# Kernel tuning notes

Measured on AMD Instinct MI355X. Metric: run time of the kernel, lower is better.

The kernel has to match this reference:

```python
import jax, jax.numpy as jnp
import numpy as np

SOS_INDEX = 1  # args.sos_index
EOS_INDEX = 2  # args.eos_index

V, H, T, B = 32000, 1024, 32, 64


def setup_inputs() -> dict:
    key = jax.random.key(0)
    ks = jax.random.split(key, 10)
    s = 0.05  # weight scale to keep softmax/tanh in a sane range
    return {
        "E": jax.random.normal(ks[0], (V, H), jnp.float32) * s,          # embedding table
        "W_ih": jax.random.normal(ks[1], (4 * H, H), jnp.float32) * s,   # LSTMCell input weights (i,f,g,o)
        "W_hh": jax.random.normal(ks[2], (4 * H, H), jnp.float32) * s,
        "b_ih": jax.random.normal(ks[3], (4 * H,), jnp.float32) * s,
        "b_hh": jax.random.normal(ks[4], (4 * H,), jnp.float32) * s,
        "W_out": jax.random.normal(ks[5], (V, H), jnp.float32) * s,      # self.out Linear
        "b_out": jnp.zeros((V,), jnp.float32),
        "encoder_hidden": jax.random.normal(ks[6], (B, H), jnp.float32),
        "encoder_cell": jax.random.normal(ks[7], (B, H), jnp.float32),
        "target_var": jax.random.randint(ks[8], (T, B), 0, V),
        "target_max_len": T,
    }


def reference(E, W_ih, W_hh, b_ih, b_hh, W_out, b_out,
              encoder_hidden, encoder_cell, target_var, target_max_len):
    # Eval-mode decode: use_teacher_forcing = False -> greedy argmax feedback.
    batch = encoder_hidden.shape[0]
    x0 = E[jnp.full((batch,), SOS_INDEX)]  # embedding(SOS) for every batch element

    def step(carry, _):
        x, h, c = carry
        # PyTorch LSTMCell: gates ordered (i, f, g, o)
        gates = x @ W_ih.T + b_ih + h @ W_hh.T + b_hh      # [B, 4H]
        i, f, g, o = jnp.split(gates, 4, axis=1)
        c_new = jax.nn.sigmoid(f) * c + jax.nn.sigmoid(i) * jnp.tanh(g)
        h_new = jax.nn.sigmoid(o) * jnp.tanh(c_new)
        logits = h_new @ W_out.T + b_out                    # [B, V]
        mask = jax.nn.softmax(logits, axis=1)[:, EOS_INDEX] # [B]
        # greedy feedback: topk(1) == argmax
        x_next = E[jnp.argmax(logits, axis=1)]              # [B, H]
        return (x_next, h_new, c_new), (logits, mask)

    _, (outputs, masks) = jax.lax.scan(
        step, (x0, encoder_hidden, encoder_cell), None, length=target_max_len)
    return outputs, masks  # [T, B, V], [T, B]
```

## Files before the change

### kernel.cpp

```cpp
#include <hip/hip_runtime.h>
#include <math.h>


typedef short bf16x8 __attribute__((ext_vector_type(8)));
typedef float f32x4 __attribute__((ext_vector_type(4)));

constexpr int kH = 1024;
constexpr int kFH = 4096;
constexpr int kB = 64;
constexpr int kV = 32000;
constexpr int kT = 32;
constexpr int kSOS = 1;
constexpr int kEOS = 2;

__device__ inline unsigned short f2bf(float f) {
  unsigned int u = __float_as_uint(f);
  u += 0x7fffu + ((u >> 16) & 1u);
  return (unsigned short)(u >> 16);
}
__device__ inline float bf2f(unsigned short h) {
  return __uint_as_float(((unsigned int)h) << 16);
}

__global__ __launch_bounds__(256) void init_kernel(
    const float* __restrict__ E, const float* __restrict__ eh,
    const float* __restrict__ ec, float* __restrict__ ws) {
  int g = blockIdx.x * 256 + threadIdx.x;
  int u = g >> 6, b = g & 63;
  float* x = ws;
  float* h = ws + 65536;
  float* c = ws + 131072;
  x[g] = E[(size_t)kSOS * kH + u];
  h[u * 64 + b] = eh[(size_t)b * kH + u];
  c[u * 64 + b] = ec[(size_t)b * kH + u];
}

__global__ __launch_bounds__(256) void wsplit_kernel(
    const float* __restrict__ W, unsigned short* __restrict__ hi,
    unsigned short* __restrict__ lo) {
  size_t i = ((size_t)blockIdx.x * 256 + threadIdx.x) * 4;
  float4 w = *(const float4*)(W + i);
  unsigned short h0 = f2bf(w.x), h1 = f2bf(w.y), h2 = f2bf(w.z), h3 = f2bf(w.w);
  ushort4 hv = make_ushort4(h0, h1, h2, h3);
  ushort4 lv = make_ushort4(f2bf(w.x - bf2f(h0)), f2bf(w.y - bf2f(h1)),
                            f2bf(w.z - bf2f(h2)), f2bf(w.w - bf2f(h3)));
  *(ushort4*)(hi + i) = hv;
  *(ushort4*)(lo + i) = lv;
}

__global__ __launch_bounds__(256) void gates_kernel(
    const float* __restrict__ Wih, const float* __restrict__ Whh,
    const float* __restrict__ x, const float* __restrict__ h,
    float* __restrict__ part) {
  __shared__ __align__(16) float Wt[64 * 68];
  __shared__ __align__(16) float Zt[64 * 68];
  const int tid = threadIdx.x;
  const int s = blockIdx.y;
  const int r0 = blockIdx.x * 64;
  const int phase = s >> 2;
  const int kc0 = (s & 3) * 256;
  const float* __restrict__ W = phase ? Whh : Wih;
  const float* __restrict__ z = phase ? h : x;
  const int tb4 = tid & 15;
  const int tr4 = tid >> 4;
  float acc[4][4];
#pragma unroll
  for (int i = 0; i < 4; ++i)
#pragma unroll
    for (int j = 0; j < 4; ++j) acc[i][j] = 0.f;

  for (int kc = kc0; kc < kc0 + 256; kc += 64) {
#pragma unroll
    for (int l = 0; l < 4; ++l) {
      int f4 = tid + 256 * l;
      int row = f4 >> 4;
      int c4 = f4 & 15;
      float4 w = *(const float4*)(W + (size_t)(r0 + row) * kH + kc + c4 * 4);
      float wv[4] = {w.x, w.y, w.z, w.w};
#pragma unroll
      for (int cc = 0; cc < 4; ++cc) {
        int c = (cc + c4) & 3;
        Wt[(c4 * 4 + c) * 68 + row] = wv[c];
      }
    }
#pragma unroll
    for (int l = 0; l < 4; ++l) {
      int f4 = tid + 256 * l;
      int kk = f4 >> 4;
      int b4 = f4 & 15;
      *(float4*)(&Zt[kk * 68 + b4 * 4]) =
          *(const float4*)(z + (size_t)(kc + kk) * 64 + b4 * 4);
    }
    __syncthreads();
#pragma unroll
    for (int kk = 0; kk < 64; ++kk) {
      float4 a = *(const float4*)(&Wt[kk * 68 + tr4 * 4]);
      float4 zb = *(const float4*)(&Zt[kk * 68 + tb4 * 4]);
      float av[4] = {a.x, a.y, a.z, a.w};
      float zv[4] = {zb.x, zb.y, zb.z, zb.w};
#pragma unroll
      for (int i = 0; i < 4; ++i)
#pragma unroll
        for (int j = 0; j < 4; ++j) acc[i][j] += av[i] * zv[j];
    }
    __syncthreads();
  }
#pragma unroll
  for (int i = 0; i < 4; ++i) {
    float4 o = make_float4(acc[i][0], acc[i][1], acc[i][2], acc[i][3]);
    *(float4*)(&part[((size_t)s * kFH + r0 + tr4 * 4 + i) * 64 + tb4 * 4]) = o;
  }
}

__global__ __launch_bounds__(256) void lstm_kernel(
    const float* __restrict__ part, const float* __restrict__ bih,
    const float* __restrict__ bhh, float* __restrict__ h,
    float* __restrict__ c, unsigned short* __restrict__ Hhi,
    unsigned short* __restrict__ Hlo) {
  int g = blockIdx.x * 256 + threadIdx.x;
  int b = g & 63, u = g >> 6;
  float gate[4];
#pragma unroll
  for (int ty = 0; ty < 4; ++ty) {
    int r = ty * kH + u;
    float acc = bih[r] + bhh[r];
#pragma unroll
    for (int s2 = 0; s2 < 8; ++s2)
      acc += part[((size_t)s2 * kFH + r) * 64 + b];
    gate[ty] = acc;
  }
  float gi = 1.f / (1.f + expf(-gate[0]));
  float gf = 1.f / (1.f + expf(-gate[1]));
  float gg = tanhf(gate[2]);
  float go = 1.f / (1.f + expf(-gate[3]));
  float cn = gf * c[g] + gi * gg;
  float hn = go * tanhf(cn);
  c[g] = cn;
  h[g] = hn;
  unsigned short hb = f2bf(hn);
  Hhi[(size_t)b * kH + u] = hb;
  Hlo[(size_t)b * kH + u] = f2bf(hn - bf2f(hb));
}

struct Frags {
  bf16x8 ah[2], al[2], bh[4], bl[4];
};

__device__ inline void load_frags(Frags& f, const unsigned short* wp0,
                                  const unsigned short* wp1,
                                  const unsigned short* lp0,
                                  const unsigned short* lp1,
                                  const unsigned short* hh,
                                  const unsigned short* hl, int ko) {
  f.ah[0] = *(const bf16x8*)(wp0 + ko);
  f.ah[1] = *(const bf16x8*)(wp1 + ko);
  f.al[0] = *(const bf16x8*)(lp0 + ko);
  f.al[1] = *(const bf16x8*)(lp1 + ko);
#pragma unroll
  for (int bt = 0; bt < 4; ++bt) {
    f.bh[bt] = *(const bf16x8*)(hh + bt * 16 * kH + ko);
    f.bl[bt] = *(const bf16x8*)(hl + bt * 16 * kH + ko);
  }
}

__device__ inline void do_mfma(const Frags& f, f32x4 acc[2][4]) {
#pragma unroll
  for (int tv = 0; tv < 2; ++tv)
#pragma unroll
    for (int bt = 0; bt < 4; ++bt) {
      acc[tv][bt] = __builtin_amdgcn_mfma_f32_16x16x32_bf16(
          f.ah[tv], f.bh[bt], acc[tv][bt], 0, 0, 0);
      acc[tv][bt] = __builtin_amdgcn_mfma_f32_16x16x32_bf16(
          f.ah[tv], f.bl[bt], acc[tv][bt], 0, 0, 0);
      acc[tv][bt] = __builtin_amdgcn_mfma_f32_16x16x32_bf16(
          f.al[tv], f.bh[bt], acc[tv][bt], 0, 0, 0);
    }
}

__global__ __launch_bounds__(256) void logits_mfma_kernel(
    const unsigned short* __restrict__ Whi, const unsigned short* __restrict__ Wlo,
    const unsigned short* __restrict__ Hhi, const unsigned short* __restrict__ Hlo,
    const float* __restrict__ bout, float* __restrict__ out,
    float* __restrict__ pmax_g, float* __restrict__ psum_g,
    int* __restrict__ pidx_g) {
  const int tid = threadIdx.x;
  const int wave = tid >> 6, lane = tid & 63;
  const int m = lane & 15, q = lane >> 4;
  const int v0 = blockIdx.x * 128 + wave * 32;
  const unsigned short* wp0 = Whi + (size_t)(v0 + m) * kH + q * 8;
  const unsigned short* wp1 = Whi + (size_t)(v0 + 16 + m) * kH + q * 8;
  const unsigned short* lp0 = Wlo + (size_t)(v0 + m) * kH + q * 8;
  const unsigned short* lp1 = Wlo + (size_t)(v0 + 16 + m) * kH + q * 8;
  const unsigned short* hh = Hhi + (size_t)m * kH + q * 8;
  const unsigned short* hl = Hlo + (size_t)m * kH + q * 8;

  f32x4 acc[2][4];
#pragma unroll
  for (int tv = 0; tv < 2; ++tv)
#pragma unroll
    for (int bt = 0; bt < 4; ++bt) acc[tv][bt] = (f32x4){0.f, 0.f, 0.f, 0.f};

  Frags f0, f1;
  load_frags(f0, wp0, wp1, lp0, lp1, hh, hl, 0);
  for (int kc = 0; kc < kH; kc += 64) {
    if (kc + 32 < kH) load_frags(f1, wp0, wp1, lp0, lp1, hh, hl, kc + 32);
    do_mfma(f0, acc);
    if (kc + 64 < kH) load_frags(f0, wp0, wp1, lp0, lp1, hh, hl, kc + 64);
    do_mfma(f1, acc);
  }

  float4 bo0 = *(const float4*)(bout + v0 + q * 4);
  float4 bo1 = *(const float4*)(bout + v0 + 16 + q * 4);
#pragma unroll
  for (int tv = 0; tv < 2; ++tv) {
    float4 bo = tv ? bo1 : bo0;
#pragma unroll
    for (int bt = 0; bt < 4; ++bt) {
      int b = bt * 16 + m;
      f32x4 a = acc[tv][bt];
      a[0] += bo.x; a[1] += bo.y; a[2] += bo.z; a[3] += bo.w;
      acc[tv][bt] = a;
      float4 o = make_float4(a[0], a[1], a[2], a[3]);
      *(float4*)(out + (size_t)b * kV + v0 + tv * 16 + q * 4) = o;
    }
  }

  __shared__ float lred[4][4][64];
  __shared__ int lidx[4][4][64];
  __shared__ float bbm[64];
  const int blk = blockIdx.x;
  const int vbase = blk * 128;

#pragma unroll
  for (int bt = 0; bt < 4; ++bt) {
    float pmv = -INFINITY;
    int piv = 0x7fffffff;
#pragma unroll
    for (int tv = 0; tv < 2; ++tv)
#pragma unroll
      for (int r = 0; r < 4; ++r) {
        float val = acc[tv][bt][r];
        int v = vbase + wave * 32 + tv * 16 + q * 4 + r;
        if (val > pmv) { pmv = val; piv = v; }
      }
    lred[wave][q][bt * 16 + m] = pmv;
    lidx[wave][q][bt * 16 + m] = piv;
  }
  __syncthreads();
  if (tid < 64) {
    float bm = -INFINITY;
    int bi = 0x7fffffff;
#pragma unroll
    for (int w = 0; w < 4; ++w)
#pragma unroll
      for (int qq = 0; qq < 4; ++qq) {
        float v2 = lred[w][qq][tid];
        int i2 = lidx[w][qq][tid];
        if (v2 > bm || (v2 == bm && i2 < bi)) { bm = v2; bi = i2; }
      }
    bbm[tid] = bm;
    pmax_g[(size_t)tid * 256 + blk] = bm;
    pidx_g[(size_t)tid * 256 + blk] = bi;
  }
  __syncthreads();
#pragma unroll
  for (int bt = 0; bt < 4; ++bt) {
    float bm = bbm[bt * 16 + m];
    float s = 0.f;
#pragma unroll
    for (int tv = 0; tv < 2; ++tv)
#pragma unroll
      for (int r = 0; r < 4; ++r) s += expf(acc[tv][bt][r] - bm);
    lred[wave][q][bt * 16 + m] = s;
  }
  __syncthreads();
  if (tid < 64) {
    float s = 0.f;
#pragma unroll
    for (int w = 0; w < 4; ++w)
#pragma unroll
      for (int qq = 0; qq < 4; ++qq) s += lred[w][qq][tid];
    psum_g[(size_t)tid * 256 + blk] = s;
  }
}

__global__ __launch_bounds__(256) void finalize_kernel(
    const float* __restrict__ pm, const float* __restrict__ ps,
    const int* __restrict__ pig, const float* __restrict__ out_t,
    const float* __restrict__ E, float* __restrict__ x,
    float* __restrict__ mask) {
  __shared__ float sm[256];
  __shared__ int si[256];
  __shared__ float ss[256];
  const int b = blockIdx.x, tid = threadIdx.x;
  float m = -INFINITY;
  int idx = 0x7fffffff;
  if (tid < 250) {
    m = pm[(size_t)b * 256 + tid];
    idx = pig[(size_t)b * 256 + tid];
  }
  sm[tid] = m;
  si[tid] = idx;
  __syncthreads();
  for (int off = 128; off > 0; off >>= 1) {
    if (tid < off) {
      float o = sm[tid + off];
      int oi = si[tid + off];
      if (o > sm[tid] || (o == sm[tid] && oi < si[tid])) {
        sm[tid] = o;
        si[tid] = oi;
      }
    }
    __syncthreads();
  }
  const float M = sm[0];
  const int amax = si[0];
  float term = 0.f;
  if (tid < 250) term = ps[(size_t)b * 256 + tid] * expf(m - M);
  ss[tid] = term;
  __syncthreads();
  for (int off = 128; off > 0; off >>= 1) {
    if (tid < off) ss[tid] += ss[tid + off];
    __syncthreads();
  }
  if (tid == 0) mask[b] = expf(out_t[(size_t)b * kV + kEOS] - M) / ss[0];
  for (int u = tid; u < kH; u += 256)
    x[(size_t)u * 64 + b] = E[(size_t)amax * kH + u];
}

extern "C" void kernel_launch(void* const* d_in, const int* in_sizes, int n_in,
                              void* d_out, int out_size, void* d_ws,
                              size_t ws_size, hipStream_t stream) {
  const float* E = (const float*)d_in[0];
  const float* Wih = (const float*)d_in[1];
  const float* Whh = (const float*)d_in[2];
  const float* bih = (const float*)d_in[3];
  const float* bhh = (const float*)d_in[4];
  const float* Wout = (const float*)d_in[5];
  const float* bout = (const float*)d_in[6];
  const float* eh = (const float*)d_in[7];
  const float* ec = (const float*)d_in[8];
  float* out = (float*)d_out;
  float* ws = (float*)d_ws;

  float* x = ws;
  float* h = ws + 65536;
  float* c = ws + 131072;
  float* part = ws + 196608;
  float* pmaxg = ws + 2293760;
  float* psumg = ws + 2310144;
  int* pidxg = (int*)(ws + 2326528);
  unsigned short* Whi = (unsigned short*)(ws + 2359296);
  unsigned short* Wlo = Whi + (size_t)kV * kH;
  unsigned short* Hhi = Wlo + (size_t)kV * kH;
  unsigned short* Hlo = Hhi + (size_t)kB * kH;

  init_kernel<<<256, 256, 0, stream>>>(E, eh, ec, ws);
  wsplit_kernel<<<kV, 256, 0, stream>>>(Wout, Whi, Wlo);
  for (int t = 0; t < kT; ++t) {
    float* out_t = out + (size_t)t * kB * kV;
    gates_kernel<<<dim3(64, 8), 256, 0, stream>>>(Wih, Whh, x, h, part);
    lstm_kernel<<<256, 256, 0, stream>>>(part, bih, bhh, h, c, Hhi, Hlo);
    logits_mfma_kernel<<<250, 256, 0, stream>>>(Whi, Wlo, Hhi, Hlo, bout,
                                                out_t, pmaxg, psumg, pidxg);
    finalize_kernel<<<64, 256, 0, stream>>>(pmaxg, psumg, pidxg, out_t, E, x,
                                            out + (size_t)kT * kB * kV + t * kB);
  }
}
```

Measured before the change: 2.972 ms.

## Fuse gate GEMM with LSTM cell and fold finalize into logits via last-block reduction

After: 5.239 ms. +76.3%, slower.

```diff
diff --git a/kernel.cpp b/kernel.cpp
--- a/kernel.cpp
+++ b/kernel.cpp
@@ -6,7 +6,6 @@
 typedef float f32x4 __attribute__((ext_vector_type(4)));
 
 constexpr int kH = 1024;
-constexpr int kFH = 4096;
 constexpr int kB = 64;
 constexpr int kV = 32000;
 constexpr int kT = 32;
@@ -23,16 +22,22 @@
 }
 
 __global__ __launch_bounds__(256) void init_kernel(
-    const float* __restrict__ E, const float* __restrict__ eh,
-    const float* __restrict__ ec, float* __restrict__ ws) {
+    const float* __restrict__ eh, const float* __restrict__ ec,
+    float* __restrict__ ws) {
   int g = blockIdx.x * 256 + threadIdx.x;
-  int u = g >> 6, b = g & 63;
-  float* x = ws;
-  float* h = ws + 65536;
-  float* c = ws + 131072;
-  x[g] = E[(size_t)kSOS * kH + u];
-  h[u * 64 + b] = eh[(size_t)b * kH + u];
-  c[u * 64 + b] = ec[(size_t)b * kH + u];
+  float* c = ws;
+  float* hT0 = ws + 65536;
+  int* counter = (int*)(ws + 245760);
+  int* amax = (int*)(ws + 245824);
+  if (g < 65536) {
+    int u = g >> 6, b = g & 63;
+    c[u * 64 + b] = ec[(size_t)b * kH + u];
+  } else {
+    int i = g - 65536;
+    hT0[i] = eh[i];
+  }
+  if (g < 64) amax[g] = kSOS;
+  if (g == 64) *counter = 0;
 }
 
 __global__ __launch_bounds__(256) void wsplit_kernel(
@@ -48,95 +53,88 @@
   *(ushort4*)(lo + i) = lv;
 }
 
-__global__ __launch_bounds__(256) void gates_kernel(
+__global__ __launch_bounds__(256) void recur_kernel(
     const float* __restrict__ Wih, const float* __restrict__ Whh,
-    const float* __restrict__ x, const float* __restrict__ h,
-    float* __restrict__ part) {
-  __shared__ __align__(16) float Wt[64 * 68];
-  __shared__ __align__(16) float Zt[64 * 68];
-  const int tid = threadIdx.x;
-  const int s = blockIdx.y;
-  const int r0 = blockIdx.x * 64;
-  const int phase = s >> 2;
-  const int kc0 = (s & 3) * 256;
-  const float* __restrict__ W = phase ? Whh : Wih;
-  const float* __restrict__ z = phase ? h : x;
-  const int tb4 = tid & 15;
-  const int tr4 = tid >> 4;
-  float acc[4][4];
-#pragma unroll
-  for (int i = 0; i < 4; ++i)
-#pragma unroll
-    for (int j = 0; j < 4; ++j) acc[i][j] = 0.f;
-
-  for (int kc = kc0; kc < kc0 + 256; kc += 64) {
-#pragma unroll
-    for (int l = 0; l < 4; ++l) {
-      int f4 = tid + 256 * l;
-      int row = f4 >> 4;
-      int c4 = f4 & 15;
-      float4 w = *(const float4*)(W + (size_t)(r0 + row) * kH + kc + c4 * 4);
-      float wv[4] = {w.x, w.y, w.z, w.w};
-#pragma unroll
-      for (int cc = 0; cc < 4; ++cc) {
-        int c = (cc + c4) & 3;
-        Wt[(c4 * 4 + c) * 68 + row] = wv[c];
-      }
-    }
-#pragma unroll
-    for (int l = 0; l < 4; ++l) {
-      int f4 = tid + 256 * l;
-      int kk = f4 >> 4;
-      int b4 = f4 & 15;
-      *(float4*)(&Zt[kk * 68 + b4 * 4]) =
-          *(const float4*)(z + (size_t)(kc + kk) * 64 + b4 * 4);
-    }
-    __syncthreads();
-#pragma unroll
-    for (int kk = 0; kk < 64; ++kk) {
-      float4 a = *(const float4*)(&Wt[kk * 68 + tr4 * 4]);
-      float4 zb = *(const float4*)(&Zt[kk * 68 + tb4 * 4]);
-      float av[4] = {a.x, a.y, a.z, a.w};
-      float zv[4] = {zb.x, zb.y, zb.z, zb.w};
-#pragma unroll
-      for (int i = 0; i < 4; ++i)
-#pragma unroll
-        for (int j = 0; j < 4; ++j) acc[i][j] += av[i] * zv[j];
-    }
-    __syncthreads();
-  }
-#pragma unroll
-  for (int i = 0; i < 4; ++i) {
-    float4 o = make_float4(acc[i][0], acc[i][1], acc[i][2], acc[i][3]);
-    *(float4*)(&part[((size_t)s * kFH + r0 + tr4 * 4 + i) * 64 + tb4 * 4]) = o;
-  }
-}
-
-__global__ __launch_bounds__(256) void lstm_kernel(
-    const float* __restrict__ part, const float* __restrict__ bih,
-    const float* __restrict__ bhh, float* __restrict__ h,
+    const float* __restrict__ E, const float* __restrict__ bih,
+    const float* __restrict__ bhh, const int* __restrict__ amax,
+    const float* __restrict__ hTprev, float* __restrict__ hTnext,
     float* __restrict__ c, unsigned short* __restrict__ Hhi,
     unsigned short* __restrict__ Hlo) {
-  int g = blockIdx.x * 256 + threadIdx.x;
-  int b = g & 63, u = g >> 6;
+  __shared__ __align__(16) float Wt[16 * 132];
+  __shared__ __align__(16) float Zt[64 * 132];
+  __shared__ const float* rowp[64];
+  const int tid = threadIdx.x;
+  const int u0 = blockIdx.x * 4;
+  const int rg = tid >> 6;
+  const int b = tid & 63;
+
+  if (tid < 64) rowp[tid] = E + (size_t)amax[tid] * kH;
+  __syncthreads();
+
+  f32x4 acc[4];
+#pragma unroll
+  for (int j = 0; j < 4; ++j) acc[j] = (f32x4){0.f, 0.f, 0.f, 0.f};
+
+  f32x4 wreg[2], zreg[8];
+  auto prefetch = [&](int cidx) {
+    const int ph = cidx >> 3;
+    const int kc = (cidx & 7) * 128;
+    const float* __restrict__ Wb = ph ? Whh : Wih;
+#pragma unroll
+    for (int l = 0; l < 2; ++l) {
+      int s = tid + 256 * l, ri = s >> 5, kq = s & 31;
+      size_t grow = (size_t)((ri >> 2) * kH + u0 + (ri & 3));
+      wreg[l] = *(const f32x4*)(Wb + grow * kH + kc + kq * 4);
+    }
+#pragma unroll
+    for (int l = 0; l < 8; ++l) {
+      int s = tid + 256 * l, zb = s >> 5, kq = s & 31;
+      const float* zp = ph ? (hTprev + (size_t)zb * kH) : rowp[zb];
+      zreg[l] = *(const f32x4*)(zp + kc + kq * 4);
+    }
+  };
+
+  prefetch(0);
+  for (int cidx = 0; cidx < 16; ++cidx) {
+#pragma unroll
+    for (int l = 0; l < 2; ++l) {
+      int s = tid + 256 * l;
+      *(f32x4*)(&Wt[(s >> 5) * 132 + (s & 31) * 4]) = wreg[l];
+    }
+#pragma unroll
+    for (int l = 0; l < 8; ++l) {
+      int s = tid + 256 * l;
+      *(f32x4*)(&Zt[(s >> 5) * 132 + (s & 31) * 4]) = zreg[l];
+    }
+    __syncthreads();
+    if (cidx < 15) prefetch(cidx + 1);
+    const float* ztb = Zt + b * 132;
+    const float* wtb = Wt + rg * 132;
+#pragma unroll
+    for (int k4 = 0; k4 < 32; ++k4) {
+      f32x4 z4 = *(const f32x4*)(ztb + k4 * 4);
+      acc[0] += (*(const f32x4*)(wtb + k4 * 4)) * z4;
+      acc[1] += (*(const f32x4*)(wtb + 528 + k4 * 4)) * z4;
+      acc[2] += (*(const f32x4*)(wtb + 1056 + k4 * 4)) * z4;
+      acc[3] += (*(const f32x4*)(wtb + 1584 + k4 * 4)) * z4;
+    }
+    __syncthreads();
+  }
+
+  const int u = u0 + rg;
   float gate[4];
 #pragma unroll
-  for (int ty = 0; ty < 4; ++ty) {
-    int r = ty * kH + u;
-    float acc = bih[r] + bhh[r];
-#pragma unroll
-    for (int s2 = 0; s2 < 8; ++s2)
-      acc += part[((size_t)s2 * kFH + r) * 64 + b];
-    gate[ty] = acc;
-  }
+  for (int j = 0; j < 4; ++j)
+    gate[j] = acc[j][0] + acc[j][1] + acc[j][2] + acc[j][3] + bih[j * kH + u] +
+              bhh[j * kH + u];
   float gi = 1.f / (1.f + expf(-gate[0]));
   float gf = 1.f / (1.f + expf(-gate[1]));
   float gg = tanhf(gate[2]);
   float go = 1.f / (1.f + expf(-gate[3]));
-  float cn = gf * c[g] + gi * gg;
+  float cn = gf * c[u * 64 + b] + gi * gg;
   float hn = go * tanhf(cn);
-  c[g] = cn;
-  h[g] = hn;
+  c[u * 64 + b] = cn;
+  hTnext[(size_t)b * kH + u] = hn;
   unsigned short hb = f2bf(hn);
   Hhi[(size_t)b * kH + u] = hb;
   Hlo[(size_t)b * kH + u] = f2bf(hn - bf2f(hb));
@@ -182,7 +180,8 @@
     const unsigned short* __restrict__ Hhi, const unsigned short* __restrict__ Hlo,
     const float* __restrict__ bout, float* __restrict__ out,
     float* __restrict__ pmax_g, float* __restrict__ psum_g,
-    int* __restrict__ pidx_g) {
+    int* __restrict__ pidx_g, int* __restrict__ counter,
+    int* __restrict__ amax_out, float* __restrict__ mask) {
   const int tid = threadIdx.x;
   const int wave = tid >> 6, lane = tid & 63;
   const int m = lane & 15, q = lane >> 4;
@@ -259,8 +258,8 @@
         if (v2 > bm || (v2 == bm && i2 < bi)) { bm = v2; bi = i2; }
       }
     bbm[tid] = bm;
-    pmax_g[(size_t)tid * 256 + blk] = bm;
-    pidx_g[(size_t)tid * 256 + blk] = bi;
+    pmax_g[(size_t)blk * 64 + tid] = bm;
+    pidx_g[(size_t)blk * 64 + tid] = bi;
   }
   __syncthreads();
 #pragma unroll
@@ -280,52 +279,57 @@
     for (int w = 0; w < 4; ++w)
 #pragma unroll
       for (int qq = 0; qq < 4; ++qq) s += lred[w][qq][tid];
-    psum_g[(size_t)tid * 256 + blk] = s;
-  }
-}
-
-__global__ __launch_bounds__(256) void finalize_kernel(
-    const float* __restrict__ pm, const float* __restrict__ ps,
-    const int* __restrict__ pig, const float* __restrict__ out_t,
-    const float* __restrict__ E, float* __restrict__ x,
-    float* __restrict__ mask) {
-  __shared__ float sm[256];
-  __shared__ int si[256];
-  __shared__ float ss[256];
-  const int b = blockIdx.x, tid = threadIdx.x;
-  float m = -INFINITY;
+    psum_g[(size_t)blk * 64 + tid] = s;
+  }
+
+  __shared__ int is_last;
+  __threadfence();
+  __syncthreads();
+  if (tid == 0) is_last = (atomicAdd(counter, 1) == 249);
+  __syncthreads();
+  if (!is_last) return;
+  __threadfence();
+
+  __shared__ float fm[4][64];
+  __shared__ int fi[4][64];
+  __shared__ float fs[4][64];
+  const int qq = tid >> 6, bb = tid & 63;
+  float mx = -INFINITY;
   int idx = 0x7fffffff;
-  if (tid < 250) {
-    m = pm[(size_t)b * 256 + tid];
-    idx = pig[(size_t)b * 256 + tid];
-  }
-  sm[tid] = m;
-  si[tid] = idx;
-  __syncthreads();
-  for (int off = 128; off > 0; off >>= 1) {
-    if (tid < off) {
-      float o = sm[tid + off];
-      int oi = si[tid + off];
-      if (o > sm[tid] || (o == sm[tid] && oi < si[tid])) {
-        sm[tid] = o;
-        si[tid] = oi;
-      }
-    }
-    __syncthreads();
-  }
-  const float M = sm[0];
-  const int amax = si[0];
-  float term = 0.f;
-  if (tid < 250) term = ps[(size_t)b * 256 + tid] * expf(m - M);
-  ss[tid] = term;
-  __syncthreads();
-  for (int off = 128; off > 0; off >>= 1) {
-    if (tid < off) ss[tid] += ss[tid + off];
-    __syncthreads();
-  }
-  if (tid == 0) mask[b] = expf(out_t[(size_t)b * kV + kEOS] - M) / ss[0];
-  for (int u = tid; u < kH; u += 256)
-    x[(size_t)u * 64 + b] = E[(size_t)amax * kH + u];
+  for (int k = qq; k < 250; k += 4) {
+    float v = pmax_g[(size_t)k * 64 + bb];
+    int ii = pidx_g[(size_t)k * 64 + bb];
+    if (v > mx || (v == mx && ii < idx)) { mx = v; idx = ii; }
+  }
+  fm[qq][bb] = mx;
+  fi[qq][bb] = idx;
+  __syncthreads();
+  if (tid < 64) {
+    float M = fm[0][tid];
+    int ai = fi[0][tid];
+#pragma unroll
+    for (int w = 1; w < 4; ++w) {
+      float v = fm[w][tid];
+      int ii = fi[w][tid];
+      if (v > M || (v == M && ii < ai)) { M = v; ai = ii; }
+    }
+    fm[0][tid] = M;
+    fi[0][tid] = ai;
+  }
+  __syncthreads();
+  float M = fm[0][bb];
+  float s = 0.f;
+  for (int k = qq; k < 250; k += 4)
+    s += psum_g[(size_t)k * 64 + bb] * expf(pmax_g[(size_t)k * 64 + bb] - M);
+  fs[qq][bb] = s;
+  __syncthreads();
+  if (tid < 64) {
+    float S = fs[0][tid] + fs[1][tid] + fs[2][tid] + fs[3][tid];
+    float eosl = out[(size_t)tid * kV + kEOS];
+    mask[tid] = expf(eosl - M) / S;
+    amax_out[tid] = fi[0][tid];
+    if (tid == 0) *counter = 0;
+  }
 }
 
 extern "C" void kernel_launch(void* const* d_in, const int* in_sizes, int n_in,
@@ -343,27 +347,29 @@
   float* out = (float*)d_out;
   float* ws = (float*)d_ws;
 
-  float* x = ws;
-  float* h = ws + 65536;
-  float* c = ws + 131072;
-  float* part = ws + 196608;
-  float* pmaxg = ws + 2293760;
-  float* psumg = ws + 2310144;
-  int* pidxg = (int*)(ws + 2326528);
+  float* c = ws;
+  float* hT0 = ws + 65536;
+  float* hT1 = ws + 131072;
+  float* pmaxg = ws + 196608;
+  float* psumg = ws + 212992;
+  int* pidxg = (int*)(ws + 229376);
+  int* counter = (int*)(ws + 245760);
+  int* amax = (int*)(ws + 245824);
   unsigned short* Whi = (unsigned short*)(ws + 2359296);
   unsigned short* Wlo = Whi + (size_t)kV * kH;
   unsigned short* Hhi = Wlo + (size_t)kV * kH;
   unsigned short* Hlo = Hhi + (size_t)kB * kH;
 
-  init_kernel<<<256, 256, 0, stream>>>(E, eh, ec, ws);
+  init_kernel<<<512, 256, 0, stream>>>(eh, ec, ws);
   wsplit_kernel<<<kV, 256, 0, stream>>>(Wout, Whi, Wlo);
   for (int t = 0; t < kT; ++t) {
     float* out_t = out + (size_t)t * kB * kV;
-    gates_kernel<<<dim3(64, 8), 256, 0, stream>>>(Wih, Whh, x, h, part);
-    lstm_kernel<<<256, 256, 0, stream>>>(part, bih, bhh, h, c, Hhi, Hlo);
-    logits_mfma_kernel<<<250, 256, 0, stream>>>(Whi, Wlo, Hhi, Hlo, bout,
-                                                out_t, pmaxg, psumg, pidxg);
-    finalize_kernel<<<64, 256, 0, stream>>>(pmaxg, psumg, pidxg, out_t, E, x,
-                                            out + (size_t)kT * kB * kV + t * kB);
-  }
-}
+    float* hTp = (t & 1) ? hT1 : hT0;
+    float* hTn = (t & 1) ? hT0 : hT1;
+    recur_kernel<<<256, 256, 0, stream>>>(Wih, Whh, E, bih, bhh, amax, hTp,
+                                          hTn, c, Hhi, Hlo);
+    logits_mfma_kernel<<<250, 256, 0, stream>>>(
+        Whi, Wlo, Hhi, Hlo, bout, out_t, pmaxg, psumg, pidxg, counter, amax,
+        out + (size_t)kT * kB * kV + t * kB);
+  }
+}
```

## Fuse argmax/mask finalize into gates kernel and stage H via LDS in logits

Applied to the files above, without the earlier changes.

Result: slower. 3.390 ms (+14.1%).

```diff
diff --git a/kernel.cpp b/kernel.cpp
--- a/kernel.cpp
+++ b/kernel.cpp
@@ -3,6 +3,7 @@
 
 
 typedef short bf16x8 __attribute__((ext_vector_type(8)));
+typedef unsigned short ush8 __attribute__((ext_vector_type(8)));
 typedef float f32x4 __attribute__((ext_vector_type(4)));
 
 constexpr int kH = 1024;
@@ -23,16 +24,19 @@
 }
 
 __global__ __launch_bounds__(256) void init_kernel(
-    const float* __restrict__ E, const float* __restrict__ eh,
-    const float* __restrict__ ec, float* __restrict__ ws) {
+    const float* __restrict__ eh, const float* __restrict__ ec,
+    float* __restrict__ ws) {
   int g = blockIdx.x * 256 + threadIdx.x;
-  int u = g >> 6, b = g & 63;
-  float* x = ws;
   float* h = ws + 65536;
   float* c = ws + 131072;
-  x[g] = E[(size_t)kSOS * kH + u];
-  h[u * 64 + b] = eh[(size_t)b * kH + u];
-  c[u * 64 + b] = ec[(size_t)b * kH + u];
+  if (g < 65536) {
+    int u = g >> 6, b = g & 63;
+    c[u * 64 + b] = ec[(size_t)b * kH + u];
+  } else {
+    int i = g - 65536;
+    int u = i >> 6, b = i & 63;
+    h[i] = eh[(size_t)b * kH + u];
+  }
 }
 
 __global__ __launch_bounds__(256) void wsplit_kernel(
@@ -50,17 +54,67 @@
 
 __global__ __launch_bounds__(256) void gates_kernel(
     const float* __restrict__ Wih, const float* __restrict__ Whh,
-    const float* __restrict__ x, const float* __restrict__ h,
-    float* __restrict__ part) {
+    const float* __restrict__ E, const float* __restrict__ h,
+    float* __restrict__ part, const float* __restrict__ pmax_g,
+    const float* __restrict__ psum_g, const int* __restrict__ pidx_g,
+    const float* __restrict__ out_prev, float* __restrict__ mask_prev, int t) {
   __shared__ __align__(16) float Wt[64 * 68];
   __shared__ __align__(16) float Zt[64 * 68];
+  __shared__ const float* rowp[64];
+  __shared__ float redA[4][64];
+  __shared__ int redI[4][64];
+  __shared__ float redS[4][64];
   const int tid = threadIdx.x;
   const int s = blockIdx.y;
   const int r0 = blockIdx.x * 64;
   const int phase = s >> 2;
   const int kc0 = (s & 3) * 256;
   const float* __restrict__ W = phase ? Whh : Wih;
-  const float* __restrict__ z = phase ? h : x;
+
+  if (!phase) {
+    const int b = tid & 63, kq = tid >> 6;
+    if (t == 0) {
+      if (tid < 64) rowp[tid] = E + (size_t)kSOS * kH;
+    } else {
+      float mx = -INFINITY;
+      int ix = 0x7fffffff;
+      for (int k = kq; k < 250; k += 4) {
+        float v = pmax_g[k * 64 + b];
+        int ii = pidx_g[k * 64 + b];
+        if (v > mx || (v == mx && ii < ix)) { mx = v; ix = ii; }
+      }
+      redA[kq][b] = mx;
+      redI[kq][b] = ix;
+      __syncthreads();
+      if (tid < 64) {
+        float M = redA[0][tid];
+        int ai = redI[0][tid];
+#pragma unroll
+        for (int w2 = 1; w2 < 4; ++w2) {
+          float v = redA[w2][tid];
+          int ii = redI[w2][tid];
+          if (v > M || (v == M && ii < ai)) { M = v; ai = ii; }
+        }
+        rowp[tid] = E + (size_t)ai * kH;
+        redA[0][tid] = M;
+      }
+      if (blockIdx.x == 0) {
+        __syncthreads();
+        float M = redA[0][b];
+        float sacc = 0.f;
+        for (int k = kq; k < 250; k += 4)
+          sacc += psum_g[k * 64 + b] * expf(pmax_g[k * 64 + b] - M);
+        redS[kq][b] = sacc;
+        __syncthreads();
+        if (tid < 64) {
+          float S = redS[0][tid] + redS[1][tid] + redS[2][tid] + redS[3][tid];
+          mask_prev[tid] = expf(out_prev[(size_t)tid * kV + kEOS] - M) / S;
+        }
+      }
+    }
+  }
+  __syncthreads();
+
   const int tb4 = tid & 15;
   const int tr4 = tid >> 4;
   float acc[4][4];
@@ -83,13 +137,24 @@
         Wt[(c4 * 4 + c) * 68 + row] = wv[c];
       }
     }
-#pragma unroll
-    for (int l = 0; l < 4; ++l) {
-      int f4 = tid + 256 * l;
-      int kk = f4 >> 4;
-      int b4 = f4 & 15;
-      *(float4*)(&Zt[kk * 68 + b4 * 4]) =
-          *(const float4*)(z + (size_t)(kc + kk) * 64 + b4 * 4);
+    if (!phase) {
+#pragma unroll
+      for (int l = 0; l < 4; ++l) {
+        int g = tid + 256 * l;
+        int zb = g >> 4, k4 = g & 15;
+        f32x4 v = *(const f32x4*)(rowp[zb] + kc + k4 * 4);
+#pragma unroll
+        for (int j = 0; j < 4; ++j) Zt[(k4 * 4 + j) * 68 + zb] = v[j];
+      }
+    } else {
+#pragma unroll
+      for (int l = 0; l < 4; ++l) {
+        int f4 = tid + 256 * l;
+        int kk = f4 >> 4;
+        int b4 = f4 & 15;
+        *(float4*)(&Zt[kk * 68 + b4 * 4]) =
+            *(const float4*)(h + (size_t)(kc + kk) * 64 + b4 * 4);
+      }
     }
     __syncthreads();
 #pragma unroll
@@ -142,47 +207,13 @@
   Hlo[(size_t)b * kH + u] = f2bf(hn - bf2f(hb));
 }
 
-struct Frags {
-  bf16x8 ah[2], al[2], bh[4], bl[4];
-};
-
-__device__ inline void load_frags(Frags& f, const unsigned short* wp0,
-                                  const unsigned short* wp1,
-                                  const unsigned short* lp0,
-                                  const unsigned short* lp1,
-                                  const unsigned short* hh,
-                                  const unsigned short* hl, int ko) {
-  f.ah[0] = *(const bf16x8*)(wp0 + ko);
-  f.ah[1] = *(const bf16x8*)(wp1 + ko);
-  f.al[0] = *(const bf16x8*)(lp0 + ko);
-  f.al[1] = *(const bf16x8*)(lp1 + ko);
-#pragma unroll
-  for (int bt = 0; bt < 4; ++bt) {
-    f.bh[bt] = *(const bf16x8*)(hh + bt * 16 * kH + ko);
-    f.bl[bt] = *(const bf16x8*)(hl + bt * 16 * kH + ko);
-  }
-}
-
-__device__ inline void do_mfma(const Frags& f, f32x4 acc[2][4]) {
-#pragma unroll
-  for (int tv = 0; tv < 2; ++tv)
-#pragma unroll
-    for (int bt = 0; bt < 4; ++bt) {
-      acc[tv][bt] = __builtin_amdgcn_mfma_f32_16x16x32_bf16(
-          f.ah[tv], f.bh[bt], acc[tv][bt], 0, 0, 0);
-      acc[tv][bt] = __builtin_amdgcn_mfma_f32_16x16x32_bf16(
-          f.ah[tv], f.bl[bt], acc[tv][bt], 0, 0, 0);
-      acc[tv][bt] = __builtin_amdgcn_mfma_f32_16x16x32_bf16(
-          f.al[tv], f.bh[bt], acc[tv][bt], 0, 0, 0);
-    }
-}
-
 __global__ __launch_bounds__(256) void logits_mfma_kernel(
     const unsigned short* __restrict__ Whi, const unsigned short* __restrict__ Wlo,
     const unsigned short* __restrict__ Hhi, const unsigned short* __restrict__ Hlo,
     const float* __restrict__ bout, float* __restrict__ out,
     float* __restrict__ pmax_g, float* __restrict__ psum_g,
     int* __restrict__ pidx_g) {
+  __shared__ __align__(16) unsigned short Hs[8192];
   const int tid = threadIdx.x;
   const int wave = tid >> 6, lane = tid & 63;
   const int m = lane & 15, q = lane >> 4;
@@ -191,8 +222,16 @@
   const unsigned short* wp1 = Whi + (size_t)(v0 + 16 + m) * kH + q * 8;
   const unsigned short* lp0 = Wlo + (size_t)(v0 + m) * kH + q * 8;
   const unsigned short* lp1 = Wlo + (size_t)(v0 + 16 + m) * kH + q * 8;
-  const unsigned short* hh = Hhi + (size_t)m * kH + q * 8;
-  const unsigned short* hl = Hlo + (size_t)m * kH + q * 8;
+
+  const unsigned short* sptr[4];
+  int sdst[4];
+#pragma unroll
+  for (int l = 0; l < 4; ++l) {
+    int g = tid + 256 * l;
+    int tile = g >> 9, row = (g >> 3) & 63, cg = g & 7;
+    sptr[l] = (tile ? Hlo : Hhi) + (size_t)row * kH + cg * 8;
+    sdst[l] = tile * 4096 + row * 64 + ((cg ^ (row & 7)) * 8);
+  }
 
   f32x4 acc[2][4];
 #pragma unroll
@@ -200,13 +239,59 @@
 #pragma unroll
     for (int bt = 0; bt < 4; ++bt) acc[tv][bt] = (f32x4){0.f, 0.f, 0.f, 0.f};
 
-  Frags f0, f1;
-  load_frags(f0, wp0, wp1, lp0, lp1, hh, hl, 0);
+  struct WF { bf16x8 ah[2], al[2]; };
+  WF w0, w1;
+  ush8 hreg[4];
+
+  auto loadW = [&](WF& f, int ko) {
+    f.ah[0] = *(const bf16x8*)(wp0 + ko);
+    f.ah[1] = *(const bf16x8*)(wp1 + ko);
+    f.al[0] = *(const bf16x8*)(lp0 + ko);
+    f.al[1] = *(const bf16x8*)(lp1 + ko);
+  };
+  auto loadH = [&](int kc) {
+#pragma unroll
+    for (int l = 0; l < 4; ++l) hreg[l] = *(const ush8*)(sptr[l] + kc);
+  };
+  auto readHfrag = [&](bf16x8 bh[4], bf16x8 bl[4], int koff) {
+    int gbase = q + (koff >> 3);
+#pragma unroll
+    for (int bt = 0; bt < 4; ++bt) {
+      int row = bt * 16 + m;
+      int off = row * 64 + ((gbase ^ (row & 7)) * 8);
+      bh[bt] = *(const bf16x8*)(Hs + off);
+      bl[bt] = *(const bf16x8*)(Hs + 4096 + off);
+    }
+  };
+  auto mfma3 = [&](const WF& f, bf16x8 bh[4], bf16x8 bl[4]) {
+#pragma unroll
+    for (int tv = 0; tv < 2; ++tv)
+#pragma unroll
+      for (int bt = 0; bt < 4; ++bt) {
+        acc[tv][bt] = __builtin_amdgcn_mfma_f32_16x16x32_bf16(
+            f.ah[tv], bh[bt], acc[tv][bt], 0, 0, 0);
+        acc[tv][bt] = __builtin_amdgcn_mfma_f32_16x16x32_bf16(
+            f.ah[tv], bl[bt], acc[tv][bt], 0, 0, 0);
+        acc[tv][bt] = __builtin_amdgcn_mfma_f32_16x16x32_bf16(
+            f.al[tv], bh[bt], acc[tv][bt], 0, 0, 0);
+      }
+  };
+
+  loadH(0);
+  loadW(w0, 0);
   for (int kc = 0; kc < kH; kc += 64) {
-    if (kc + 32 < kH) load_frags(f1, wp0, wp1, lp0, lp1, hh, hl, kc + 32);
-    do_mfma(f0, acc);
-    if (kc + 64 < kH) load_frags(f0, wp0, wp1, lp0, lp1, hh, hl, kc + 64);
-    do_mfma(f1, acc);
+    __syncthreads();
+#pragma unroll
+    for (int l = 0; l < 4; ++l) *(ush8*)(Hs + sdst[l]) = hreg[l];
+    __syncthreads();
+    if (kc + 64 < kH) loadH(kc + 64);
+    bf16x8 bh[4], bl[4];
+    loadW(w1, kc + 32);
+    readHfrag(bh, bl, 0);
+    mfma3(w0, bh, bl);
+    if (kc + 64 < kH) loadW(w0, kc + 64);
+    readHfrag(bh, bl, 32);
+    mfma3(w1, bh, bl);
   }
 
   float4 bo0 = *(const float4*)(bout + v0 + q * 4);
@@ -259,8 +344,8 @@
         if (v2 > bm || (v2 == bm && i2 < bi)) { bm = v2; bi = i2; }
       }
     bbm[tid] = bm;
-    pmax_g[(size_t)tid * 256 + blk] = bm;
-    pidx_g[(size_t)tid * 256 + blk] = bi;
+    pmax_g[(size_t)blk * 64 + tid] = bm;
+    pidx_g[(size_t)blk * 64 + tid] = bi;
   }
   __syncthreads();
 #pragma unroll
@@ -280,52 +365,39 @@
     for (int w = 0; w < 4; ++w)
 #pragma unroll
       for (int qq = 0; qq < 4; ++qq) s += lred[w][qq][tid];
-    psum_g[(size_t)tid * 256 + blk] = s;
-  }
-}
-
-__global__ __launch_bounds__(256) void finalize_kernel(
+    psum_g[(size_t)blk * 64 + tid] = s;
+  }
+}
+
+__global__ __launch_bounds__(256) void final_mask_kernel(
     const float* __restrict__ pm, const float* __restrict__ ps,
-    const int* __restrict__ pig, const float* __restrict__ out_t,
-    const float* __restrict__ E, float* __restrict__ x,
-    float* __restrict__ mask) {
-  __shared__ float sm[256];
-  __shared__ int si[256];
-  __shared__ float ss[256];
-  const int b = blockIdx.x, tid = threadIdx.x;
-  float m = -INFINITY;
-  int idx = 0x7fffffff;
-  if (tid < 250) {
-    m = pm[(size_t)b * 256 + tid];
-    idx = pig[(size_t)b * 256 + tid];
-  }
-  sm[tid] = m;
-  si[tid] = idx;
-  __syncthreads();
-  for (int off = 128; off > 0; off >>= 1) {
-    if (tid < off) {
-      float o = sm[tid + off];
-      int oi = si[tid + off];
-      if (o > sm[tid] || (o == sm[tid] && oi < si[tid])) {
-        sm[tid] = o;
-        si[tid] = oi;
-      }
-    }
-    __syncthreads();
-  }
-  const float M = sm[0];
-  const int amax = si[0];
-  float term = 0.f;
-  if (tid < 250) term = ps[(size_t)b * 256 + tid] * expf(m - M);
-  ss[tid] = term;
-  __syncthreads();
-  for (int off = 128; off > 0; off >>= 1) {
-    if (tid < off) ss[tid] += ss[tid + off];
-    __syncthreads();
-  }
-  if (tid == 0) mask[b] = expf(out_t[(size_t)b * kV + kEOS] - M) / ss[0];
-  for (int u = tid; u < kH; u += 256)
-    x[(size_t)u * 64 + b] = E[(size_t)amax * kH + u];
+    const float* __restrict__ out_t, float* __restrict__ mask) {
+  __shared__ float rm[4][64];
+  __shared__ float rs[4][64];
+  const int tid = threadIdx.x;
+  const int b = tid & 63, kq = tid >> 6;
+  float mx = -INFINITY;
+  for (int k = kq; k < 250; k += 4) {
+    float v = pm[k * 64 + b];
+    if (v > mx) mx = v;
+  }
+  rm[kq][b] = mx;
+  __syncthreads();
+  if (tid < 64) {
+    float M = fmaxf(fmaxf(rm[0][tid], rm[1][tid]), fmaxf(rm[2][tid], rm[3][tid]));
+    rm[0][tid] = M;
+  }
+  __syncthreads();
+  float M = rm[0][b];
+  float s = 0.f;
+  for (int k = kq; k < 250; k += 4)
+    s += ps[k * 64 + b] * expf(pm[k * 64 + b] - M);
+  rs[kq][b] = s;
+  __syncthreads();
+  if (tid < 64) {
+    float S = rs[0][tid] + rs[1][tid] + rs[2][tid] + rs[3][tid];
+    mask[tid] = expf(out_t[(size_t)tid * kV + kEOS] - M) / S;
+  }
 }
 
 extern "C" void kernel_launch(void* const* d_in, const int* in_sizes, int n_in,
@@ -343,7 +415,6 @@
   float* out = (float*)d_out;
   float* ws = (float*)d_ws;
 
-  float* x = ws;
   float* h = ws + 65536;
   float* c = ws + 131072;
   float* part = ws + 196608;
@@ -354,16 +425,21 @@
   unsigned short* Wlo = Whi + (size_t)kV * kH;
   unsigned short* Hhi = Wlo + (size_t)kV * kH;
   unsigned short* Hlo = Hhi + (size_t)kB * kH;
-
-  init_kernel<<<256, 256, 0, stream>>>(E, eh, ec, ws);
+  float* maskbase = out + (size_t)kT * kB * kV;
+
+  init_kernel<<<512, 256, 0, stream>>>(eh, ec, ws);
   wsplit_kernel<<<kV, 256, 0, stream>>>(Wout, Whi, Wlo);
   for (int t = 0; t < kT; ++t) {
     float* out_t = out + (size_t)t * kB * kV;
-    gates_kernel<<<dim3(64, 8), 256, 0, stream>>>(Wih, Whh, x, h, part);
+    const float* out_prev = t ? out + (size_t)(t - 1) * kB * kV : nullptr;
+    float* mask_prev = t ? maskbase + (size_t)(t - 1) * kB : nullptr;
+    gates_kernel<<<dim3(64, 8), 256, 0, stream>>>(
+        Wih, Whh, E, h, part, pmaxg, psumg, pidxg, out_prev, mask_prev, t);
     lstm_kernel<<<256, 256, 0, stream>>>(part, bih, bhh, h, c, Hhi, Hlo);
     logits_mfma_kernel<<<250, 256, 0, stream>>>(Whi, Wlo, Hhi, Hlo, bout,
                                                 out_t, pmaxg, psumg, pidxg);
-    finalize_kernel<<<64, 256, 0, stream>>>(pmaxg, psumg, pidxg, out_t, E, x,
-                                            out + (size_t)kT * kB * kV + t * kB);
-  }
-}
+  }
+  final_mask_kernel<<<1, 256, 0, stream>>>(
+      pmaxg, psumg, out + (size_t)(kT - 1) * kB * kV,
+      maskbase + (size_t)(kT - 1) * kB);
+}
```

## Split logits K dimension across two wave groups with LDS reduction

Applied to the files above, without the earlier changes.

After: 3.001 ms. About the same (+1.0%).

```diff
diff --git a/kernel.cpp b/kernel.cpp
--- a/kernel.cpp
+++ b/kernel.cpp
@@ -177,7 +177,7 @@
     }
 }
 
-__global__ __launch_bounds__(256) void logits_mfma_kernel(
+__global__ __launch_bounds__(512, 2) void logits_mfma_kernel(
     const unsigned short* __restrict__ Whi, const unsigned short* __restrict__ Wlo,
     const unsigned short* __restrict__ Hhi, const unsigned short* __restrict__ Hlo,
     const float* __restrict__ bout, float* __restrict__ out,
@@ -185,14 +185,17 @@
     int* __restrict__ pidx_g) {
   const int tid = threadIdx.x;
   const int wave = tid >> 6, lane = tid & 63;
+  const int ws = wave & 3;
+  const int kh = wave >> 2;
   const int m = lane & 15, q = lane >> 4;
-  const int v0 = blockIdx.x * 128 + wave * 32;
-  const unsigned short* wp0 = Whi + (size_t)(v0 + m) * kH + q * 8;
-  const unsigned short* wp1 = Whi + (size_t)(v0 + 16 + m) * kH + q * 8;
-  const unsigned short* lp0 = Wlo + (size_t)(v0 + m) * kH + q * 8;
-  const unsigned short* lp1 = Wlo + (size_t)(v0 + 16 + m) * kH + q * 8;
-  const unsigned short* hh = Hhi + (size_t)m * kH + q * 8;
-  const unsigned short* hl = Hlo + (size_t)m * kH + q * 8;
+  const int v0 = blockIdx.x * 128 + ws * 32;
+  const int koff = kh * 512;
+  const unsigned short* wp0 = Whi + (size_t)(v0 + m) * kH + koff + q * 8;
+  const unsigned short* wp1 = Whi + (size_t)(v0 + 16 + m) * kH + koff + q * 8;
+  const unsigned short* lp0 = Wlo + (size_t)(v0 + m) * kH + koff + q * 8;
+  const unsigned short* lp1 = Wlo + (size_t)(v0 + 16 + m) * kH + koff + q * 8;
+  const unsigned short* hh = Hhi + (size_t)m * kH + koff + q * 8;
+  const unsigned short* hl = Hlo + (size_t)m * kH + koff + q * 8;
 
   f32x4 acc[2][4];
 #pragma unroll
@@ -202,26 +205,49 @@
 
   Frags f0, f1;
   load_frags(f0, wp0, wp1, lp0, lp1, hh, hl, 0);
-  for (int kc = 0; kc < kH; kc += 64) {
-    if (kc + 32 < kH) load_frags(f1, wp0, wp1, lp0, lp1, hh, hl, kc + 32);
+  for (int kc = 0; kc < 512; kc += 64) {
+    if (kc + 32 < 512) load_frags(f1, wp0, wp1, lp0, lp1, hh, hl, kc + 32);
     do_mfma(f0, acc);
-    if (kc + 64 < kH) load_frags(f0, wp0, wp1, lp0, lp1, hh, hl, kc + 64);
+    if (kc + 64 < 512) load_frags(f0, wp0, wp1, lp0, lp1, hh, hl, kc + 64);
     do_mfma(f1, acc);
   }
 
-  float4 bo0 = *(const float4*)(bout + v0 + q * 4);
-  float4 bo1 = *(const float4*)(bout + v0 + 16 + q * 4);
-#pragma unroll
-  for (int tv = 0; tv < 2; ++tv) {
-    float4 bo = tv ? bo1 : bo0;
-#pragma unroll
-    for (int bt = 0; bt < 4; ++bt) {
-      int b = bt * 16 + m;
-      f32x4 a = acc[tv][bt];
-      a[0] += bo.x; a[1] += bo.y; a[2] += bo.z; a[3] += bo.w;
-      acc[tv][bt] = a;
-      float4 o = make_float4(a[0], a[1], a[2], a[3]);
-      *(float4*)(out + (size_t)b * kV + v0 + tv * 16 + q * 4) = o;
+  __shared__ float combf[4][32][65];
+  if (kh == 1) {
+#pragma unroll
+    for (int tv = 0; tv < 2; ++tv)
+#pragma unroll
+      for (int bt = 0; bt < 4; ++bt)
+#pragma unroll
+        for (int r = 0; r < 4; ++r)
+          combf[ws][(tv * 4 + bt) * 4 + r][lane] = acc[tv][bt][r];
+  }
+  __syncthreads();
+  if (kh == 0) {
+#pragma unroll
+    for (int tv = 0; tv < 2; ++tv)
+#pragma unroll
+      for (int bt = 0; bt < 4; ++bt)
+#pragma unroll
+        for (int r = 0; r < 4; ++r)
+          acc[tv][bt][r] += combf[ws][(tv * 4 + bt) * 4 + r][lane];
+  }
+
+  if (kh == 0) {
+    float4 bo0 = *(const float4*)(bout + v0 + q * 4);
+    float4 bo1 = *(const float4*)(bout + v0 + 16 + q * 4);
+#pragma unroll
+    for (int tv = 0; tv < 2; ++tv) {
+      float4 bo = tv ? bo1 : bo0;
+#pragma unroll
+      for (int bt = 0; bt < 4; ++bt) {
+        int b = bt * 16 + m;
+        f32x4 a = acc[tv][bt];
+        a[0] += bo.x; a[1] += bo.y; a[2] += bo.z; a[3] += bo.w;
+        acc[tv][bt] = a;
+        float4 o = make_float4(a[0], a[1], a[2], a[3]);
+        *(float4*)(out + (size_t)b * kV + v0 + tv * 16 + q * 4) = o;
+      }
     }
   }
 
@@ -231,20 +257,22 @@
   const int blk = blockIdx.x;
   const int vbase = blk * 128;
 
-#pragma unroll
-  for (int bt = 0; bt < 4; ++bt) {
-    float pmv = -INFINITY;
-    int piv = 0x7fffffff;
-#pragma unroll
-    for (int tv = 0; tv < 2; ++tv)
-#pragma unroll
-      for (int r = 0; r < 4; ++r) {
-        float val = acc[tv][bt][r];
-        int v = vbase + wave * 32 + tv * 16 + q * 4 + r;
-        if (val > pmv) { pmv = val; piv = v; }
-      }
-    lred[wave][q][bt * 16 + m] = pmv;
-    lidx[wave][q][bt * 16 + m] = piv;
+  if (kh == 0) {
+#pragma unroll
+    for (int bt = 0; bt < 4; ++bt) {
+      float pmv = -INFINITY;
+      int piv = 0x7fffffff;
+#pragma unroll
+      for (int tv = 0; tv < 2; ++tv)
+#pragma unroll
+        for (int r = 0; r < 4; ++r) {
+          float val = acc[tv][bt][r];
+          int v = vbase + ws * 32 + tv * 16 + q * 4 + r;
+          if (val > pmv) { pmv = val; piv = v; }
+        }
+      lred[ws][q][bt * 16 + m] = pmv;
+      lidx[ws][q][bt * 16 + m] = piv;
+    }
   }
   __syncthreads();
   if (tid < 64) {
@@ -263,15 +291,17 @@
     pidx_g[(size_t)tid * 256 + blk] = bi;
   }
   __syncthreads();
-#pragma unroll
-  for (int bt = 0; bt < 4; ++bt) {
-    float bm = bbm[bt * 16 + m];
-    float s = 0.f;
-#pragma unroll
-    for (int tv = 0; tv < 2; ++tv)
-#pragma unroll
-      for (int r = 0; r < 4; ++r) s += expf(acc[tv][bt][r] - bm);
-    lred[wave][q][bt * 16 + m] = s;
+  if (kh == 0) {
+#pragma unroll
+    for (int bt = 0; bt < 4; ++bt) {
+      float bm = bbm[bt * 16 + m];
+      float s = 0.f;
+#pragma unroll
+      for (int tv = 0; tv < 2; ++tv)
+#pragma unroll
+        for (int r = 0; r < 4; ++r) s += expf(acc[tv][bt][r] - bm);
+      lred[ws][q][bt * 16 + m] = s;
+    }
   }
   __syncthreads();
   if (tid < 64) {
@@ -325,7 +355,7 @@
   }
   if (tid == 0) mask[b] = expf(out_t[(size_t)b * kV + kEOS] - M) / ss[0];
   for (int u = tid; u < kH; u += 256)
-    x[(size_t)u * 64 + b] = E[(size_t)amax * kH + u];
+    x[u * 64 + b] = E[(size_t)amax * kH + u];
 }
 
 extern "C" void kernel_launch(void* const* d_in, const int* in_sizes, int n_in,
@@ -361,8 +391,8 @@
     float* out_t = out + (size_t)t * kB * kV;
     gates_kernel<<<dim3(64, 8), 256, 0, stream>>>(Wih, Whh, x, h, part);
     lstm_kernel<<<256, 256, 0, stream>>>(part, bih, bhh, h, c, Hhi, Hlo);
-    logits_mfma_kernel<<<250, 256, 0, stream>>>(Whi, Wlo, Hhi, Hlo, bout,
-                                                out_t, pmaxg, psumg, pidxg);
+    logits_mfma_kernel<<<250, 512, 0, stream>>>(
+        Whi, Wlo, Hhi, Hlo, bout, out_t, pmaxg, psumg, pidxg);
     finalize_kernel<<<64, 256, 0, stream>>>(pmaxg, psumg, pidxg, out_t, E, x,
                                             out + (size_t)kT * kB * kV + t * kB);
   }
```
